# Optimization experiments

Measured on AMD Instinct MI355X. Metric: run time of the kernel, lower is better.

The kernel has to match this reference:

```python
import jax, jax.numpy as jnp
import numpy as np

NUM_ANTENNAS = 16
D = 0.5
WAVELENGTH = 1.0
RHO = 0.8


def setup_inputs() -> dict:
    key = jax.random.key(0)
    k = jax.random.split(key, 5)
    return {
        "W": jax.random.normal(k[0], (2_000_000, 2 * NUM_ANTENNAS), dtype=jnp.float32),
        "Hc_real": jax.random.normal(k[1], (4, 8, NUM_ANTENNAS), dtype=jnp.float32),
        "Hc_imag": jax.random.normal(k[2], (4, 8, NUM_ANTENNAS), dtype=jnp.float32),
        "Hs_real": jax.random.normal(k[3], (4, 4, NUM_ANTENNAS), dtype=jnp.float32),
        "Hs_imag": jax.random.normal(k[4], (4, 4, NUM_ANTENNAS), dtype=jnp.float32),
    }


def _estimate_angles(h_real, h_imag):
    """Vectorized version of the per-(b,t) phase-unwrap + OLS slope fit.

    h_real/h_imag: [B, T, N] -> angles [B, T] in degrees.
    """
    n = jnp.arange(NUM_ANTENNAS, dtype=h_real.dtype)
    phases = jnp.arctan2(h_imag, h_real)                      # torch.angle
    pd = jnp.diff(phases, axis=-1)
    pd = (pd + jnp.pi) % (2.0 * jnp.pi) - jnp.pi              # wrap to (-pi, pi]
    zeros = jnp.zeros(phases.shape[:-1] + (1,), phases.dtype)
    unwrapped = jnp.concatenate([zeros, jnp.cumsum(pd, axis=-1)], axis=-1)  # [B,T,N]
    # OLS slope of unwrapped vs n (closed form of solve(XtX, XtY) with X=[n,1])
    n_c = n - n.mean()
    slope = (unwrapped * n_c).sum(-1) / (n_c * n_c).sum()     # [B,T]
    sin_theta = jnp.clip(slope * WAVELENGTH / (2.0 * jnp.pi * D), -1.0, 1.0)
    return -jnp.rad2deg(jnp.arcsin(sin_theta))


def _steering_phase(angles_deg):
    # phase[t, n] = 2*pi*d*n*sin(theta_t)/wavelength  -> [T, N]
    n = jnp.arange(NUM_ANTENNAS, dtype=angles_deg.dtype)
    s = jnp.sin(jnp.deg2rad(angles_deg))
    return 2.0 * jnp.pi * D * s[:, None] * n[None, :] / WAVELENGTH


def reference(W, Hc_real, Hc_imag, Hs_real, Hs_imag):
    user_angles = _estimate_angles(Hc_real, Hc_imag)[0]       # [Tc]
    target_angles = _estimate_angles(Hs_real, Hs_imag)[0]     # [Ts]

    Wr = W[:, :NUM_ANTENNAS]
    Wi = W[:, NUM_ANTENNAS:]

    def gains(phase):  # |w_cplx @ conj(sv).T|, all-real math
        c = jnp.cos(phase)  # [T, N]
        s = jnp.sin(phase)
        re = Wr @ c.T + Wi @ s.T  # [B, T]
        im = Wi @ c.T - Wr @ s.T
        return jnp.sqrt(re * re + im * im)

    user_gains = gains(_steering_phase(user_angles))          # [B, Tc]
    target_gains = gains(_steering_phase(target_angles))      # [B, Ts]

    min_user_gain = user_gains.min(axis=1)
    sum_user_gain = user_gains.sum(axis=1)
    avg_target_gain = target_gains.mean(axis=1)

    comm_loss = -RHO * 2.5 * (min_user_gain + 0.1 * sum_user_gain)
    sens_loss = -(1.0 - RHO) * avg_target_gain
    return jnp.mean(comm_loss + sens_loss)
```

## Files before the change

### kernel.cpp

```cpp
#include <hip/hip_runtime.h>
#include <math.h>

#define NA 16
#define NBEAM 12
#define NUSER 8

#define ACC_OFFSET 1536

__global__ void mtl_angles_kernel(const float* __restrict__ Hc_r, const float* __restrict__ Hc_i,
                                  const float* __restrict__ Hs_r, const float* __restrict__ Hs_i,
                                  float* __restrict__ table, double* __restrict__ acc) {
    int t = threadIdx.x;
    if (t == 0) *acc = 0.0;
    if (t >= NBEAM) return;

    const float* re;
    const float* im;
    if (t < NUSER) { re = Hc_r + t * NA;           im = Hc_i + t * NA; }
    else           { re = Hs_r + (t - NUSER) * NA; im = Hs_i + (t - NUSER) * NA; }

    const float PI_F   = 3.14159265358979323846f;
    const float TWO_PI = 6.28318530717958647692f;

    float ph[NA];
    #pragma unroll
    for (int n = 0; n < NA; ++n) ph[n] = atan2f(im[n], re[n]);

    float unw = 0.f, dotsum = 0.f;
    #pragma unroll
    for (int n = 1; n < NA; ++n) {
        float pd = ph[n] - ph[n - 1];
        float x  = pd + PI_F;
        float m  = fmodf(x, TWO_PI);
        if (m < 0.f) m += TWO_PI;
        pd = m - PI_F;
        unw += pd;
        dotsum += unw * ((float)n - 7.5f);
    }
    float slope = dotsum / 340.0f;
    float sin_theta = slope / PI_F;
    sin_theta = fminf(1.0f, fmaxf(-1.0f, sin_theta));
    float st = -sin_theta;

    #pragma unroll
    for (int n = 0; n < NA; ++n) {
        float phase = PI_F * st * (float)n;
        table[t * 2 * NA + n]      = cosf(phase);
        table[t * 2 * NA + NA + n] = sinf(phase);
    }
}

__device__ __forceinline__ float dot4(float4 a, float4 b) {
    return a.x * b.x + a.y * b.y + a.z * b.z + a.w * b.w;
}

__device__ __forceinline__ void load_lds16(const float* g, float* l) {
    __builtin_amdgcn_global_load_lds(
        (const __attribute__((address_space(1))) void*)g,
        (__attribute__((address_space(3))) void*)l, 16, 0, 0);
}

__device__ __forceinline__ float row_loss(const float4* w, const float* tbs) {
    float minU = 3.4e38f, sumU = 0.f, sumT = 0.f;
    #pragma unroll 1
    for (int j = 0; j < NBEAM; ++j) {
        const float4* tc = (const float4*)(tbs + j * 32);
        float re = 0.f, im = 0.f;
        #pragma unroll
        for (int q = 0; q < 4; ++q) {
            float4 c = tc[q], s = tc[q + 4];
            float4 wr = w[q], wi = w[q + 4];
            re += dot4(wr, c) + dot4(wi, s);
            im += dot4(wi, c) - dot4(wr, s);
        }
        float g = sqrtf(re * re + im * im);
        if (j < NUSER) { minU = fminf(minU, g); sumU += g; }
        else           { sumT += g; }
    }
    return -2.0f * (minU + 0.1f * sumU) - 0.05f * sumT;
}

__global__ __launch_bounds__(256, 2) void mtl_gains_kernel(const float* __restrict__ W,
                                                           const float* __restrict__ table,
                                                           double* __restrict__ acc, int rows) {
    __shared__ float sh[4 * 2 * 2048];
    __shared__ float tbs[NBEAM * 2 * NA];
    __shared__ float wsum[4];

    const int t = threadIdx.x;
    for (int i = t; i < NBEAM * 2 * NA; i += blockDim.x) tbs[i] = table[i];
    __syncthreads();

    const int wid  = t >> 6;
    const int lane = t & 63;
    float* buf0 = sh + wid * 4096;
    float* buf1 = buf0 + 2048;

    const int sq      = (lane & 7) ^ ((lane >> 3) & 7);
    const int src_off = (lane >> 3) * 32 + sq * 4;

    const int ntiles    = rows >> 6;
    const int nwaves    = gridDim.x * 4;
    const int gw        = blockIdx.x * 4 + wid;
    const int base_cnt  = ntiles / nwaves;
    const int rem       = ntiles % nwaves;
    const int t0        = gw * base_cnt + (gw < rem ? gw : rem);
    const int t1        = t0 + base_cnt + (gw < rem ? 1 : 0);

    float local = 0.f;

    if (t0 < t1) {
        {
            const float* src = W + (size_t)t0 * 2048 + src_off;
            #pragma unroll
            for (int k = 0; k < 8; ++k) load_lds16(src + k * 256, buf0 + k * 256);
        }
        #pragma unroll 1
        for (int tt = t0; tt < t1; ++tt) {
            float* cur = ((tt - t0) & 1) ? buf1 : buf0;
            float* nxt = ((tt - t0) & 1) ? buf0 : buf1;
            if (tt + 1 < t1) {
                const float* src = W + (size_t)(tt + 1) * 2048 + src_off;
                #pragma unroll
                for (int k = 0; k < 8; ++k) load_lds16(src + k * 256, nxt + k * 256);
                asm volatile("s_waitcnt vmcnt(8)" ::: "memory");
            } else {
                asm volatile("s_waitcnt vmcnt(0)" ::: "memory");
            }

            const float* myrow = cur + lane * 32;
            float4 w[8];
            #pragma unroll
            for (int q = 0; q < 8; ++q) {
                int s = q ^ (lane & 7);
                w[q] = *(const float4*)(myrow + s * 4);
            }
            local += row_loss(w, tbs);
        }
    }

    int tailbase = ntiles << 6;
    if (blockIdx.x == 0) {
        int row = tailbase + t;
        if (row < rows) {
            const float4* wp = (const float4*)(W + (size_t)row * 32);
            float4 w[8];
            #pragma unroll
            for (int i = 0; i < 8; ++i) w[i] = wp[i];
            local += row_loss(w, tbs);
        }
    }

    #pragma unroll
    for (int off = 32; off > 0; off >>= 1) local += __shfl_down(local, off);
    if (lane == 0) wsum[wid] = local;
    __syncthreads();
    if (t == 0) {
        float b = wsum[0] + wsum[1] + wsum[2] + wsum[3];
        atomicAdd(acc, (double)b);
    }
}

__global__ void mtl_finalize_kernel(const double* __restrict__ acc, float* __restrict__ out, int rows) {
    if (threadIdx.x == 0) out[0] = (float)(*acc / (double)rows);
}

extern "C" void kernel_launch(void* const* d_in, const int* in_sizes, int n_in,
                              void* d_out, int out_size, void* d_ws, size_t ws_size,
                              hipStream_t stream) {
    const float* W    = (const float*)d_in[0];
    const float* Hc_r = (const float*)d_in[1];
    const float* Hc_i = (const float*)d_in[2];
    const float* Hs_r = (const float*)d_in[3];
    const float* Hs_i = (const float*)d_in[4];
    float* out = (float*)d_out;

    int rows = in_sizes[0] / (2 * NA);
    float*  table = (float*)d_ws;
    double* acc   = (double*)((char*)d_ws + ACC_OFFSET);

    mtl_angles_kernel<<<1, 64, 0, stream>>>(Hc_r, Hc_i, Hs_r, Hs_i, table, acc);

    mtl_gains_kernel<<<512, 256, 0, stream>>>(W, table, acc, rows);

    mtl_finalize_kernel<<<1, 64, 0, stream>>>(acc, out, rows);
}
```

Measured before the change: 376.6 us.

## Split beams across half-waves, halve LDS tiles, fuse finalize via last-block atomic

Each wave now processes 32-row tiles, with the two half-waves each computing 6 of the 12 beams for the same row and combining partial min/sums with xor shuffles. This halves the per-wave LDS buffer, so four blocks can be resident per CU and the grid doubles to 1024 blocks, aiming for more memory-level parallelism on a bandwidth-bound stream of W. The separate finalize kernel is removed: the last block to finish, detected via an atomic counter, writes the mean. The cost is redundant W register loads per row and the extra shuffles.

```diff
diff --git a/kernel.cpp b/kernel.cpp
--- a/kernel.cpp
+++ b/kernel.cpp
@@ -9,9 +9,10 @@
 
 __global__ void mtl_angles_kernel(const float* __restrict__ Hc_r, const float* __restrict__ Hc_i,
                                   const float* __restrict__ Hs_r, const float* __restrict__ Hs_i,
-                                  float* __restrict__ table, double* __restrict__ acc) {
+                                  float* __restrict__ table, double* __restrict__ acc,
+                                  unsigned* __restrict__ done) {
     int t = threadIdx.x;
-    if (t == 0) *acc = 0.0;
+    if (t == 0) { *acc = 0.0; *done = 0u; }
     if (t >= NBEAM) return;
 
     const float* re;
@@ -80,10 +81,12 @@
     return -2.0f * (minU + 0.1f * sumU) - 0.05f * sumT;
 }
 
-__global__ __launch_bounds__(256, 2) void mtl_gains_kernel(const float* __restrict__ W,
+__global__ __launch_bounds__(256, 4) void mtl_gains_kernel(const float* __restrict__ W,
                                                            const float* __restrict__ table,
-                                                           double* __restrict__ acc, int rows) {
-    __shared__ float sh[4 * 2 * 2048];
+                                                           double* __restrict__ acc,
+                                                           unsigned* __restrict__ done,
+                                                           float* __restrict__ out, int rows) {
+    __shared__ float sh[4 * 2 * 1024];
     __shared__ float tbs[NBEAM * 2 * NA];
     __shared__ float wsum[4];
 
@@ -93,57 +96,84 @@
 
     const int wid  = t >> 6;
     const int lane = t & 63;
-    float* buf0 = sh + wid * 4096;
-    float* buf1 = buf0 + 2048;
+    float* buf0 = sh + wid * 2048;
+    float* buf1 = buf0 + 1024;
 
     const int sq      = (lane & 7) ^ ((lane >> 3) & 7);
     const int src_off = (lane >> 3) * 32 + sq * 4;
 
-    const int ntiles    = rows >> 6;
-    const int nwaves    = gridDim.x * 4;
-    const int gw        = blockIdx.x * 4 + wid;
-    const int base_cnt  = ntiles / nwaves;
-    const int rem       = ntiles % nwaves;
-    const int t0        = gw * base_cnt + (gw < rem ? gw : rem);
-    const int t1        = t0 + base_cnt + (gw < rem ? 1 : 0);
+    const int ntiles = rows >> 5;
+    const int nwaves = gridDim.x * 4;
+    const int gw     = blockIdx.x * 4 + wid;
+    const int cnt    = ntiles / nwaves;
+    const int rem    = ntiles % nwaves;
+    const int t0     = gw * cnt + (gw < rem ? gw : rem);
+    const int t1     = t0 + cnt + (gw < rem ? 1 : 0);
+
+    const int h      = lane >> 5;
+    const int row    = lane & 31;
+    const int jbase  = h * 6;
+    const float* tb  = tbs + jbase * 2 * NA;
 
     float local = 0.f;
 
     if (t0 < t1) {
         {
-            const float* src = W + (size_t)t0 * 2048 + src_off;
+            const float* src = W + (size_t)t0 * 1024 + src_off;
             #pragma unroll
-            for (int k = 0; k < 8; ++k) load_lds16(src + k * 256, buf0 + k * 256);
+            for (int k = 0; k < 4; ++k) load_lds16(src + k * 256, buf0 + k * 256);
         }
         #pragma unroll 1
         for (int tt = t0; tt < t1; ++tt) {
             float* cur = ((tt - t0) & 1) ? buf1 : buf0;
             float* nxt = ((tt - t0) & 1) ? buf0 : buf1;
             if (tt + 1 < t1) {
-                const float* src = W + (size_t)(tt + 1) * 2048 + src_off;
+                const float* src = W + (size_t)(tt + 1) * 1024 + src_off;
                 #pragma unroll
-                for (int k = 0; k < 8; ++k) load_lds16(src + k * 256, nxt + k * 256);
-                asm volatile("s_waitcnt vmcnt(8)" ::: "memory");
+                for (int k = 0; k < 4; ++k) load_lds16(src + k * 256, nxt + k * 256);
+                asm volatile("s_waitcnt vmcnt(4)" ::: "memory");
             } else {
                 asm volatile("s_waitcnt vmcnt(0)" ::: "memory");
             }
 
-            const float* myrow = cur + lane * 32;
+            const float* myrow = cur + row * 32;
             float4 w[8];
             #pragma unroll
             for (int q = 0; q < 8; ++q) {
-                int s = q ^ (lane & 7);
+                int s = q ^ (row & 7);
                 w[q] = *(const float4*)(myrow + s * 4);
             }
-            local += row_loss(w, tbs);
-        }
-    }
-
-    int tailbase = ntiles << 6;
+
+            float minU = 3.4e38f, sumU = 0.f, sumT = 0.f;
+            #pragma unroll 1
+            for (int jj = 0; jj < 6; ++jj) {
+                const float4* tc = (const float4*)(tb + jj * 32);
+                float re = 0.f, im = 0.f;
+                #pragma unroll
+                for (int q = 0; q < 4; ++q) {
+                    float4 c = tc[q], s = tc[q + 4];
+                    float4 wr = w[q], wi = w[q + 4];
+                    re += dot4(wr, c) + dot4(wi, s);
+                    im += dot4(wi, c) - dot4(wr, s);
+                }
+                float g = sqrtf(re * re + im * im);
+                bool isU = (jbase + jj) < NUSER;
+                minU = isU ? fminf(minU, g) : minU;
+                sumU += isU ? g : 0.f;
+                sumT += isU ? 0.f : g;
+            }
+            minU = fminf(minU, __shfl_xor(minU, 32));
+            sumU += __shfl_xor(sumU, 32);
+            sumT += __shfl_xor(sumT, 32);
+            local += 0.5f * (-2.0f * (minU + 0.1f * sumU) - 0.05f * sumT);
+        }
+    }
+
+    int tailbase = ntiles << 5;
     if (blockIdx.x == 0) {
-        int row = tailbase + t;
-        if (row < rows) {
-            const float4* wp = (const float4*)(W + (size_t)row * 32);
+        int r = tailbase + t;
+        if (r < rows) {
+            const float4* wp = (const float4*)(W + (size_t)r * 32);
             float4 w[8];
             #pragma unroll
             for (int i = 0; i < 8; ++i) w[i] = wp[i];
@@ -158,11 +188,13 @@
     if (t == 0) {
         float b = wsum[0] + wsum[1] + wsum[2] + wsum[3];
         atomicAdd(acc, (double)b);
-    }
-}
-
-__global__ void mtl_finalize_kernel(const double* __restrict__ acc, float* __restrict__ out, int rows) {
-    if (threadIdx.x == 0) out[0] = (float)(*acc / (double)rows);
+        __threadfence();
+        unsigned prev = atomicAdd(done, 1u);
+        if (prev == gridDim.x - 1) {
+            double total = atomicAdd(acc, 0.0);
+            out[0] = (float)(total / (double)rows);
+        }
+    }
 }
 
 extern "C" void kernel_launch(void* const* d_in, const int* in_sizes, int n_in,
@@ -176,12 +208,11 @@
     float* out = (float*)d_out;
 
     int rows = in_sizes[0] / (2 * NA);
-    float*  table = (float*)d_ws;
-    double* acc   = (double*)((char*)d_ws + ACC_OFFSET);
-
-    mtl_angles_kernel<<<1, 64, 0, stream>>>(Hc_r, Hc_i, Hs_r, Hs_i, table, acc);
-
-    mtl_gains_kernel<<<512, 256, 0, stream>>>(W, table, acc, rows);
-
-    mtl_finalize_kernel<<<1, 64, 0, stream>>>(acc, out, rows);
-}
+    float*    table = (float*)d_ws;
+    double*   acc   = (double*)((char*)d_ws + ACC_OFFSET);
+    unsigned* done  = (unsigned*)((char*)d_ws + ACC_OFFSET + 8);
+
+    mtl_angles_kernel<<<1, 64, 0, stream>>>(Hc_r, Hc_i, Hs_r, Hs_i, table, acc, done);
+
+    mtl_gains_kernel<<<1024, 256, 0, stream>>>(W, table, acc, done, out, rows);
+}
```

Result: slower. 408.4 us (+8.4%).
